# Performance work log

Hardware: AMD Instinct MI355X
Metric: run time of the kernel (lower is better)

Reference implementation:

```python
import jax, jax.numpy as jnp
import numpy as np

STRIDES = [8, 16, 32, 64, 128]
FSIZES = [64, 32, 16, 8, 4]          # 512x512 input
NUM_CLASSES = 80
POS_THR, NEG_THR = 0.5, 0.4          # MaxIOUAssigner thresholds
BETA = 1.0 / 9.0                      # SmoothL1 beta (from loss_bbox cfg)
BBOX_W = 10.0                         # SmoothL1 loss_weight
ALPHA, GAMMA = 0.25, 2.0              # sigmoid focal loss


def _gen_anchors():
    """RetinaNet-style grid anchors, xyxy, concatenated over levels -> [A,4]."""
    ratios = np.array([0.5, 1.0, 2.0])
    scales = 4.0 * 2.0 ** (np.arange(3) / 3.0)   # octave_base_scale=4, 3 octaves
    levels = []
    for s, f in zip(STRIDES, FSIZES):
        ws = (s * scales[None, :] / np.sqrt(ratios)[:, None]).reshape(-1)  # [9]
        hs = (s * scales[None, :] * np.sqrt(ratios)[:, None]).reshape(-1)
        c = (np.arange(f) + 0.5) * s
        sx, sy = np.meshgrid(c, c)
        cxy = np.stack([sx, sy], -1).reshape(-1, 1, 2)   # [f*f,1,2]
        wh = np.stack([ws, hs], -1)[None]                # [1,9,2]
        a = np.concatenate([cxy - wh / 2, cxy + wh / 2], -1).reshape(-1, 4)
        levels.append(a)
    return jnp.asarray(np.concatenate(levels, 0), dtype=jnp.float32)  # [49104,4]


def _iou(anchors, gt):  # [A,4],[M,4] -> [A,M]
    area_a = (anchors[:, 2] - anchors[:, 0]) * (anchors[:, 3] - anchors[:, 1])
    area_g = (gt[:, 2] - gt[:, 0]) * (gt[:, 3] - gt[:, 1])
    lt = jnp.maximum(anchors[:, None, :2], gt[None, :, :2])
    rb = jnp.minimum(anchors[:, None, 2:], gt[None, :, 2:])
    wh = jnp.clip(rb - lt, 0.0)
    inter = wh[..., 0] * wh[..., 1]
    return inter / jnp.maximum(area_a[:, None] + area_g[None, :] - inter, 1e-6)


def _encode(boxes, anchors):  # DeltaXYWH encode, target_stds = 1
    aw = anchors[:, 2] - anchors[:, 0]
    ah = anchors[:, 3] - anchors[:, 1]
    ax = (anchors[:, 0] + anchors[:, 2]) * 0.5
    ay = (anchors[:, 1] + anchors[:, 3]) * 0.5
    gw = jnp.maximum(boxes[:, 2] - boxes[:, 0], 1e-6)
    gh = jnp.maximum(boxes[:, 3] - boxes[:, 1], 1e-6)
    gx = (boxes[:, 0] + boxes[:, 2]) * 0.5
    gy = (boxes[:, 1] + boxes[:, 3]) * 0.5
    return jnp.stack([(gx - ax) / aw, (gy - ay) / ah,
                      jnp.log(gw / aw), jnp.log(gh / ah)], -1)


def _assign_one(gt_boxes, gt_labels, gt_mask, anchors):
    """Per-image: IoU match, pseudo-sample, gather matched GT, encode, masks."""
    iou = _iou(anchors, gt_boxes)                      # [A,M]
    iou = jnp.where(gt_mask[None, :], iou, -1.0)       # kill padded GTs
    best = jnp.argmax(iou, 1)                          # [A]
    best_iou = jnp.max(iou, 1)
    # matched index: >=0 matched, -1 background, -2 ignored
    idx = jnp.where(best_iou >= POS_THR, best,
                    jnp.where(best_iou < NEG_THR, -1, -2))
    pos = idx >= 0
    matched = jnp.where(pos[:, None], gt_boxes[best], 0.0)   # gather_based_on_match
    reg_t = _encode(matched, anchors)
    total = jnp.maximum(1.0, jnp.sum(pos.astype(jnp.float32)))
    mask_reg = pos.astype(jnp.float32)[:, None] / total      # [A,1] -> broadcast 4
    labels = jnp.where(pos, gt_labels[best], -1)             # bg/ignored -> -1
    mask_cls = (idx >= -1).astype(jnp.float32) / total       # matched + background
    return reg_t, mask_reg, labels, mask_cls


def setup_inputs() -> dict:
    key = jax.random.key(0)
    ks = jax.random.split(key, 6)
    B, M, A, C = 16, 100, 49104, NUM_CLASSES
    cls_score = jax.random.normal(ks[0], (B, A, C), jnp.float32)
    bbox_pred = jax.random.normal(ks[1], (B, A, 4), jnp.float32) * 0.1
    cxy = jax.random.uniform(ks[2], (B, M, 2), jnp.float32, 50.0, 462.0)
    wh = jax.random.uniform(ks[3], (B, M, 2), jnp.float32, 16.0, 128.0)
    target_boxes = jnp.concatenate([cxy - wh / 2, cxy + wh / 2], -1)
    target_labels = jax.random.randint(ks[4], (B, M), 0, C, jnp.int32)
    mask_labels = jax.random.randint(ks[5], (B, M), 0, 2, jnp.int32).astype(bool)
    return {"cls_score": cls_score, "bbox_pred": bbox_pred,
            "target_boxes": target_boxes, "target_labels": target_labels,
            "mask_labels": mask_labels}


def reference(cls_score, bbox_pred, target_boxes, target_labels, mask_labels):
    anchors = _gen_anchors()                                        # [A,4]
    reg_t, mask_reg, labels, mask_cls = jax.vmap(
        _assign_one, in_axes=(0, 0, 0, None))(
        target_boxes, target_labels, mask_labels, anchors)          # per image
    bs = float(cls_score.shape[0])
    # SmoothL1 (beta=1/9, weight 10), masked + normalized per image
    d = jnp.abs(bbox_pred - reg_t)
    l1 = jnp.where(d < BETA, 0.5 * d * d / BETA, d - 0.5 * BETA)
    loss_bbox = BBOX_W * jnp.sum(l1 * mask_reg) / bs
    # sigmoid focal loss
    t = jax.nn.one_hot(labels, NUM_CLASSES, dtype=cls_score.dtype)  # -1 -> all-zero
    bce = t * jax.nn.softplus(-cls_score) + (1.0 - t) * jax.nn.softplus(cls_score)
    p = jax.nn.sigmoid(cls_score)
    pt = t * p + (1.0 - t) * (1.0 - p)
    at = ALPHA * t + (1.0 - ALPHA) * (1.0 - t)
    focal = at * (1.0 - pt) ** GAMMA * bce
    loss_cls = jnp.sum(focal * mask_cls[..., None]) / bs
    return jnp.stack([loss_cls, loss_bbox])
```

## Files before the change

### kernel.cpp

```cpp
#include <hip/hip_runtime.h>

#define N_ANCH 49104
#define NB_IMG 16
#define NGT 100
#define NC 80
#define BPI 96
#define APB 512
#define NBLK (BPI * NB_IMG)
#define ROW_F4 (NC / 4)
#define MAXG 104

#define LOG2E 1.4426950408889634f
#define LN2   0.6931471805599453f
#define FSCALE (0.75f * LN2)

__constant__ float BW9[9] = {
  (float)(4.0               / 0.7071067811865476 * 0.5),
  (float)(5.039684199579493 / 0.7071067811865476 * 0.5),
  (float)(6.349604207872798 / 0.7071067811865476 * 0.5),
  (float)(4.0               * 0.5),
  (float)(5.039684199579493 * 0.5),
  (float)(6.349604207872798 * 0.5),
  (float)(4.0               / 1.4142135623730951 * 0.5),
  (float)(5.039684199579493 / 1.4142135623730951 * 0.5),
  (float)(6.349604207872798 / 1.4142135623730951 * 0.5),
};
__constant__ float BH9[9] = {
  (float)(4.0               * 0.7071067811865476 * 0.5),
  (float)(5.039684199579493 * 0.7071067811865476 * 0.5),
  (float)(6.349604207872798 * 0.7071067811865476 * 0.5),
  (float)(4.0               * 0.5),
  (float)(5.039684199579493 * 0.5),
  (float)(6.349604207872798 * 0.5),
  (float)(4.0               * 1.4142135623730951 * 0.5),
  (float)(5.039684199579493 * 1.4142135623730951 * 0.5),
  (float)(6.349604207872798 * 1.4142135623730951 * 0.5),
};

__device__ __forceinline__ float frcp(float x){ return __builtin_amdgcn_rcpf(x); }
__device__ __forceinline__ float fexp2(float x){ return __builtin_amdgcn_exp2f(x); }
__device__ __forceinline__ float flog2(float x){ return __builtin_amdgcn_logf(x); }

__device__ __forceinline__ float f0_term(float x){
  float xl = x * LOG2E;
  float mx = fmaxf(xl, 0.f);
  float mn = fminf(xl, 0.f);
  float u  = fexp2(mn - mx);
  float w  = 1.0f + u;
  float lw = flog2(w);
  float g  = mn - lw;
  return fexp2(g + g) * (lw + mx);
}
__device__ __forceinline__ float f0x4(float4 c4){
  return (f0_term(c4.x) + f0_term(c4.y)) + (f0_term(c4.z) + f0_term(c4.w));
}

__device__ __forceinline__ float corr_term(float x){
  float xl = x * LOG2E;
  float mx = fmaxf(xl, 0.f);
  float mn = fminf(xl, 0.f);
  float u  = fexp2(mn - mx);
  float w  = 1.0f + u;
  float lw = flog2(w);
  float p2   = fexp2(2.f * (mn - lw));
  float omp2 = fexp2(-2.f * (mx + lw));
  float sp   = LN2 * (lw + mx);
  float spn  = LN2 * (lw - mn);
  return 0.25f * omp2 * spn - 0.75f * p2 * sp;
}

__device__ __forceinline__ void anchor_geom(int a, float& x1, float& y1,
                                            float& x2, float& y2){
  int lg, st, rel;
  if      (a < 36864){ lg = 6; st = 8;   rel = a; }
  else if (a < 46080){ lg = 5; st = 16;  rel = a - 36864; }
  else if (a < 48384){ lg = 4; st = 32;  rel = a - 46080; }
  else if (a < 48960){ lg = 3; st = 64;  rel = a - 48384; }
  else               { lg = 2; st = 128; rel = a - 48960; }
  int cell = rel / 9;
  int k    = rel - cell * 9;
  int yy   = cell >> lg;
  int xx   = cell & ((1 << lg) - 1);
  float stf = (float)st;
  float cx = ((float)xx + 0.5f) * stf;
  float cy = ((float)yy + 0.5f) * stf;
  float w2 = stf * BW9[k];
  float h2 = stf * BH9[k];
  x1 = cx - w2; y1 = cy - h2; x2 = cx + w2; y2 = cy + h2;
}

__global__ __launch_bounds__(256, 6) void fused_loss_kernel(
    const float* __restrict__ cls,
    const float* __restrict__ bbox,
    const float* __restrict__ gtb,
    const int*   __restrict__ gtl,
    const unsigned char* __restrict__ gmask,
    float* __restrict__ ws)
{
  const int tid = threadIdx.x;
  const int wv = tid >> 6, ln = tid & 63;
  const int b  = blockIdx.y;
  const int a0 = blockIdx.x * APB;
  const int bid = b * BPI + blockIdx.x;
  const int nvalid = min(N_ANCH - a0, APB);
  const int nf4 = nvalid * ROW_F4;

  __shared__ float4 s_cgt[4][MAXG];
  __shared__ float  s_carea[4][MAXG];
  __shared__ int    s_clab[4][MAXG];
  __shared__ float  s_wf[APB];
  __shared__ float  s_r0[4], s_r1[4], s_r2[4];

  const float* clsbase = cls + (size_t)(b * N_ANCH + a0) * NC;
  const float4* cp = (const float4*)clsbase;

  float4 pf0 = cp[tid];
  float4 pf1 = cp[tid + 256];

  float ax1[2], ay1[2], ax2[2], ay2[2];
  #pragma unroll
  for (int r = 0; r < 2; ++r){
    int a = a0 + r * 256 + tid;
    if (a < N_ANCH) anchor_geom(a, ax1[r], ay1[r], ax2[r], ay2[r]);
    else { ax1[r] = 0.f; ay1[r] = 3.0e38f; ax2[r] = 0.f; ay2[r] = -3.0e38f; }
  }

  float ymin = fminf(ay1[0], ay1[1]);
  float ymax = fmaxf(ay2[0], ay2[1]);
  #pragma unroll
  for (int o = 32; o > 0; o >>= 1){
    ymin = fminf(ymin, __shfl_xor(ymin, o));
    ymax = fmaxf(ymax, __shfl_xor(ymax, o));
  }

  const unsigned int* mw = (const unsigned int*)gmask;
  bool nfb = false, ob = false;
  for (int i = ln; i < (NB_IMG * NGT) / 4; i += 64){
    unsigned int w = mw[i];
    nfb |= (w != 0u && w != 0x3F800000u);
    ob  |= ((w & 0xFFFFFF00u) != 0u);
  }
  const bool byteLayout = __any((int)nfb) && __any((int)ob);

  const float4* g4 = (const float4*)gtb;
  float4 g = g4[b * NGT + ln];
  int v = byteLayout ? (gmask[b * NGT + ln] != 0)
                     : (((const unsigned int*)gmask)[b * NGT + ln] != 0u);
  bool pass = v && (g.y < ymax) && (g.w > ymin);
  unsigned long long bal = __ballot(pass);
  int pre = __popcll(bal & ((1ull << ln) - 1ull));
  if (pass){
    s_cgt[wv][pre]   = g;
    s_carea[wv][pre] = (g.z - g.x) * (g.w - g.y);
    s_clab[wv][pre]  = gtl[b * NGT + ln];
  }
  int cnt = __popcll(bal);
  float4 g1; bool pass1 = false;
  if (ln < NGT - 64){
    g1 = g4[b * NGT + 64 + ln];
    int v1 = byteLayout ? (gmask[b * NGT + 64 + ln] != 0)
                        : (((const unsigned int*)gmask)[b * NGT + 64 + ln] != 0u);
    pass1 = v1 && (g1.y < ymax) && (g1.w > ymin);
  }
  unsigned long long bal1 = __ballot(pass1);
  int pre1 = cnt + __popcll(bal1 & ((1ull << ln) - 1ull));
  if (pass1){
    s_cgt[wv][pre1]   = g1;
    s_carea[wv][pre1] = (g1.z - g1.x) * (g1.w - g1.y);
    s_clab[wv][pre1]  = gtl[b * NGT + 64 + ln];
  }
  cnt += __popcll(bal1);
  if (ln == 0){
    float4 far4; far4.x = 3e9f; far4.y = 3e9f; far4.z = 3e9f; far4.w = 3e9f;
    s_cgt[wv][cnt]   = far4; s_carea[wv][cnt]   = 0.f; s_clab[wv][cnt]   = 0;
    s_cgt[wv][cnt+1] = far4; s_carea[wv][cnt+1] = 0.f; s_clab[wv][cnt+1] = 0;
  }
  const int cntp = (cnt + 1) & ~1;

  float accB = 0.f, posf = 0.f, fcorr = 0.f;
  #pragma unroll
  for (int r = 0; r < 2; ++r){
    int row = r * 256 + tid;
    int a = a0 + row;
    float x1 = ax1[r], y1 = ay1[r], x2 = ax2[r], y2 = ay2[r];
    float areaA = (x2 - x1) * (y2 - y1);
    float Ib = -1.f, Ub = 1.f; int best = 0;
    for (int j = 0; j < cntp; j += 2){
      #pragma unroll
      for (int u2 = 0; u2 < 2; ++u2){
        int jj = j + u2;
        float4 gg = s_cgt[wv][jj];
        float lx = fmaxf(x1, gg.x), ly = fmaxf(y1, gg.y);
        float rx = fminf(x2, gg.z), ry = fminf(y2, gg.w);
        float iw = fmaxf(rx - lx, 0.f), ih = fmaxf(ry - ly, 0.f);
        float I  = iw * ih;
        float U  = (areaA + s_carea[wv][jj]) - I;
        bool gt = I * Ub > Ib * U;
        best = gt ? jj : best;
        Ib = gt ? I : Ib;
        Ub = gt ? U : Ub;
      }
    }
    bool va  = a < N_ANCH;
    bool pos = va && (2.f * Ib >= Ub);
    bool ign = va && !pos && (5.f * Ib >= 2.f * Ub);
    s_wf[row] = ign ? 0.f : 1.f;

    if (pos){
      posf += 1.f;
      float4 gg = s_cgt[wv][best];
      float aw = x2 - x1, ah = y2 - y1;
      float axc = (x1 + x2) * 0.5f, ayc = (y1 + y2) * 0.5f;
      float gw = fmaxf(gg.z - gg.x, 1e-6f), gh = fmaxf(gg.w - gg.y, 1e-6f);
      float gxc = (gg.x + gg.z) * 0.5f, gyc = (gg.y + gg.w) * 0.5f;
      float t0 = (gxc - axc) / aw, t1 = (gyc - ayc) / ah;
      float t2 = LN2 * flog2(gw * frcp(aw));
      float t3 = LN2 * flog2(gh * frcp(ah));
      float4 bp = ((const float4*)bbox)[(size_t)b * N_ANCH + a];
      const float BETA = 1.0f / 9.0f;
      float d0 = fabsf(bp.x - t0), d1 = fabsf(bp.y - t1);
      float d2 = fabsf(bp.z - t2), d3 = fabsf(bp.w - t3);
      accB += (d0 < BETA) ? 4.5f * d0 * d0 : d0 - 0.5f * BETA;
      accB += (d1 < BETA) ? 4.5f * d1 * d1 : d1 - 0.5f * BETA;
      accB += (d2 < BETA) ? 4.5f * d2 * d2 : d2 - 0.5f * BETA;
      accB += (d3 < BETA) ? 4.5f * d3 * d3 : d3 - 0.5f * BETA;
      int lab = s_clab[wv][best];
      fcorr += corr_term(clsbase[(size_t)row * NC + lab]);
    }
  }
  __syncthreads();

  float fraw = 0.f;
  fraw = fmaf(s_wf[tid / 20],         f0x4(pf0), fraw);
  fraw = fmaf(s_wf[(tid + 256) / 20], f0x4(pf1), fraw);
  for (int i = tid + 512; i < nf4; i += 256){
    float4 c4 = cp[i];
    fraw = fmaf(s_wf[i / 20], f0x4(c4), fraw);
  }
  float accC = fmaf(FSCALE, fraw, fcorr);

  #pragma unroll
  for (int o = 32; o > 0; o >>= 1){
    accC += __shfl_down(accC, o);
    accB += __shfl_down(accB, o);
    posf += __shfl_down(posf, o);
  }
  if (ln == 0){ s_r0[wv] = accC; s_r1[wv] = accB; s_r2[wv] = posf; }
  __syncthreads();
  if (tid == 0){
    ws[bid]            = s_r0[0] + s_r0[1] + s_r0[2] + s_r0[3];
    ws[NBLK + bid]     = s_r1[0] + s_r1[1] + s_r1[2] + s_r1[3];
    ws[2 * NBLK + bid] = s_r2[0] + s_r2[1] + s_r2[2] + s_r2[3];
  }
}

__global__ void finalize_kernel(const float* __restrict__ ws,
                                float* __restrict__ out)
{
  __shared__ float sC[NB_IMG], sB[NB_IMG];
  const int tid = threadIdx.x;
  const int wv = tid >> 6, ln = tid & 63;
  #pragma unroll
  for (int i = 0; i < 2; ++i){
    int b = wv * 2 + i;
    float c = 0.f, bb = 0.f, p = 0.f;
    for (int k = ln; k < BPI; k += 64){
      c  += ws[b * BPI + k];
      bb += ws[NBLK + b * BPI + k];
      p  += ws[2 * NBLK + b * BPI + k];
    }
    #pragma unroll
    for (int o = 32; o > 0; o >>= 1){
      c += __shfl_down(c, o); bb += __shfl_down(bb, o); p += __shfl_down(p, o);
    }
    if (ln == 0){
      float tot = fmaxf(p, 1.f);
      sC[b] = c / tot;
      sB[b] = bb / tot;
    }
  }
  __syncthreads();
  if (tid == 0){
    float lc = 0.f, lb = 0.f;
    #pragma unroll
    for (int b = 0; b < NB_IMG; ++b){ lc += sC[b]; lb += sB[b]; }
    out[0] = lc / 16.f;
    out[1] = 10.f * lb / 16.f;
  }
}

extern "C" void kernel_launch(void* const* d_in, const int* in_sizes, int n_in,
                              void* d_out, int out_size, void* d_ws, size_t ws_size,
                              hipStream_t stream) {
  const float* cls  = (const float*)d_in[0];
  const float* bbox = (const float*)d_in[1];
  const float* gtb  = (const float*)d_in[2];
  const int*   gtl  = (const int*)d_in[3];
  const unsigned char* gmask = (const unsigned char*)d_in[4];

  float* ws = (float*)d_ws;

  dim3 grid(BPI, NB_IMG);
  fused_loss_kernel<<<grid, 256, 0, stream>>>(cls, bbox, gtb, gtl, gmask, ws);
  finalize_kernel<<<1, 512, 0, stream>>>(ws, (float*)d_out);
}
```

Measured before the change: 56.17 us.

## Partition anchor rows per wavefront to drop block barrier and deepen prefetch

Each wavefront now owns a contiguous 128-row slice of the block's anchors, for both IoU assignment and the focal-loss sweep. Per-row weights in shared memory are then produced and consumed by the same wave, so the block-wide __syncthreads before the classification pass is removed. The change also prefetches six float4 loads per lane before the assignment work instead of two, and unrolls the streaming loop into four independent loads and accumulators for more memory-level parallelism. In exchange, register pressure rises under the existing launch bounds, and the anchor-to-lane mapping changes coalescing for the bbox and geometry accesses.

```diff
diff --git a/kernel.cpp b/kernel.cpp
--- a/kernel.cpp
+++ b/kernel.cpp
@@ -6,9 +6,12 @@
 #define NC 80
 #define BPI 96
 #define APB 512
+#define RPW 128
 #define NBLK (BPI * NB_IMG)
 #define ROW_F4 (NC / 4)
+#define WCH (RPW * ROW_F4)
 #define MAXG 104
+#define NPF 6
 
 #define LOG2E 1.4426950408889634f
 #define LN2   0.6931471805599453f
@@ -104,6 +107,9 @@
   const int bid = b * BPI + blockIdx.x;
   const int nvalid = min(N_ANCH - a0, APB);
   const int nf4 = nvalid * ROW_F4;
+  const int wb  = wv * WCH;
+  const int jend = min(WCH, nf4 - wb);
+  const int rbase = wv * RPW;
 
   __shared__ float4 s_cgt[4][MAXG];
   __shared__ float  s_carea[4][MAXG];
@@ -114,13 +120,14 @@
   const float* clsbase = cls + (size_t)(b * N_ANCH + a0) * NC;
   const float4* cp = (const float4*)clsbase;
 
-  float4 pf0 = cp[tid];
-  float4 pf1 = cp[tid + 256];
+  float4 pf[NPF];
+  #pragma unroll
+  for (int k = 0; k < NPF; ++k) pf[k] = cp[wb + ln + k * 64];
 
   float ax1[2], ay1[2], ax2[2], ay2[2];
   #pragma unroll
   for (int r = 0; r < 2; ++r){
-    int a = a0 + r * 256 + tid;
+    int a = a0 + rbase + 2 * ln + r;
     if (a < N_ANCH) anchor_geom(a, ax1[r], ay1[r], ax2[r], ay2[r]);
     else { ax1[r] = 0.f; ay1[r] = 3.0e38f; ax2[r] = 0.f; ay2[r] = -3.0e38f; }
   }
@@ -180,7 +187,7 @@
   float accB = 0.f, posf = 0.f, fcorr = 0.f;
   #pragma unroll
   for (int r = 0; r < 2; ++r){
-    int row = r * 256 + tid;
+    int row = rbase + 2 * ln + r;
     int a = a0 + row;
     float x1 = ax1[r], y1 = ay1[r], x2 = ax2[r], y2 = ay2[r];
     float areaA = (x2 - x1) * (y2 - y1);
@@ -228,16 +235,31 @@
       fcorr += corr_term(clsbase[(size_t)row * NC + lab]);
     }
   }
-  __syncthreads();
-
-  float fraw = 0.f;
-  fraw = fmaf(s_wf[tid / 20],         f0x4(pf0), fraw);
-  fraw = fmaf(s_wf[(tid + 256) / 20], f0x4(pf1), fraw);
-  for (int i = tid + 512; i < nf4; i += 256){
-    float4 c4 = cp[i];
-    fraw = fmaf(s_wf[i / 20], f0x4(c4), fraw);
-  }
-  float accC = fmaf(FSCALE, fraw, fcorr);
+
+  float fr0 = 0.f, fr1 = 0.f, fr2 = 0.f, fr3 = 0.f;
+  #pragma unroll
+  for (int k = 0; k < NPF; ++k){
+    int j = ln + k * 64;
+    float t = fmaf(s_wf[rbase + j / 20], f0x4(pf[k]), 0.f);
+    if ((k & 3) == 0) fr0 += t; else if ((k & 3) == 1) fr1 += t;
+    else if ((k & 3) == 2) fr2 += t; else fr3 += t;
+  }
+  int j = NPF * 64 + ln;
+  for (; j + 192 < jend; j += 256){
+    float4 c0 = cp[wb + j];
+    float4 c1 = cp[wb + j + 64];
+    float4 c2 = cp[wb + j + 128];
+    float4 c3 = cp[wb + j + 192];
+    fr0 = fmaf(s_wf[rbase + j / 20],         f0x4(c0), fr0);
+    fr1 = fmaf(s_wf[rbase + (j + 64) / 20],  f0x4(c1), fr1);
+    fr2 = fmaf(s_wf[rbase + (j + 128) / 20], f0x4(c2), fr2);
+    fr3 = fmaf(s_wf[rbase + (j + 192) / 20], f0x4(c3), fr3);
+  }
+  for (; j < jend; j += 64){
+    float4 c4 = cp[wb + j];
+    fr0 = fmaf(s_wf[rbase + j / 20], f0x4(c4), fr0);
+  }
+  float accC = fmaf(FSCALE, (fr0 + fr1) + (fr2 + fr3), fcorr);
 
   #pragma unroll
   for (int o = 32; o > 0; o >>= 1){
```

Measured after the change: 53.33 us, median of 2. 5.0% less time.
